# Optimization experiments

Hardware: AMD Instinct MI355X
Metric: run time of the kernel (lower is better)

## Reference

```python
import jax, jax.numpy as jnp
import numpy as np

B, R, H, IN, L = 8, 128, 256, 512, 3
NH, DH = 4, H // 4  # attention heads


def _layernorm(x, g, b, eps=1e-5):
    mu = jnp.mean(x, axis=-1, keepdims=True)
    var = jnp.mean(jnp.square(x - mu), axis=-1, keepdims=True)
    return (x - mu) * jax.lax.rsqrt(var + eps) * g + b


def setup_inputs() -> dict:
    key = jax.random.key(0)
    ks = iter(jax.random.split(key, 40))
    s = 0.02
    d = {}
    d['x'] = jax.random.normal(next(ks), (B, IN), jnp.float32)
    d['We'] = jax.random.normal(next(ks), (IN, H), jnp.float32) * s
    d['be'] = jnp.zeros((H,), jnp.float32)
    # per-graph-layer params, stacked along leading L axis
    d['msg_W1'] = jax.random.normal(next(ks), (L, 2 * H, H), jnp.float32) * s
    d['msg_b1'] = jnp.zeros((L, H), jnp.float32)
    d['msg_W2'] = jax.random.normal(next(ks), (L, H, H), jnp.float32) * s
    d['msg_b2'] = jnp.zeros((L, H), jnp.float32)
    d['upd_W1'] = jax.random.normal(next(ks), (L, 2 * H, H), jnp.float32) * s
    d['upd_b1'] = jnp.zeros((L, H), jnp.float32)
    d['upd_W2'] = jax.random.normal(next(ks), (L, H, H), jnp.float32) * s
    d['upd_b2'] = jnp.zeros((L, H), jnp.float32)
    d['ln_g'] = jnp.ones((L, H), jnp.float32)
    d['ln_b'] = jnp.zeros((L, H), jnp.float32)
    d['rule_adj'] = jax.random.normal(next(ks), (R, R), jnp.float32)
    # multihead attention (4 heads)
    d['Wq'] = jax.random.normal(next(ks), (H, H), jnp.float32) * s
    d['bq'] = jnp.zeros((H,), jnp.float32)
    d['Wk'] = jax.random.normal(next(ks), (H, H), jnp.float32) * s
    d['bk'] = jnp.zeros((H,), jnp.float32)
    d['Wv'] = jax.random.normal(next(ks), (H, H), jnp.float32) * s
    d['bv'] = jnp.zeros((H,), jnp.float32)
    d['Wo'] = jax.random.normal(next(ks), (H, H), jnp.float32) * s
    d['bo'] = jnp.zeros((H,), jnp.float32)
    # readout MLP -> num_rules logits
    d['ro_W1'] = jax.random.normal(next(ks), (H, H), jnp.float32) * s
    d['ro_b1'] = jnp.zeros((H,), jnp.float32)
    d['ro_W2'] = jax.random.normal(next(ks), (H, R), jnp.float32) * s
    d['ro_b2'] = jnp.zeros((R,), jnp.float32)
    return d


def reference(x, We, be, msg_W1, msg_b1, msg_W2, msg_b2,
              upd_W1, upd_b1, upd_W2, upd_b2, ln_g, ln_b, rule_adj,
              Wq, bq, Wk, bk, Wv, bv, Wo, bo,
              ro_W1, ro_b1, ro_W2, ro_b2):
    # node encoder, broadcast to all rule-graph nodes: [B,R,H]
    h0 = x @ We + be
    h = jnp.broadcast_to(h0[:, None, :], (B, R, H))
    # rule adjacency with self-edges excluded (loop used i != j)
    A = jax.nn.sigmoid(rule_adj) * (1.0 - jnp.eye(R, dtype=rule_adj.dtype))  # [R,R]
    for l in range(L):
        # message_net(cat(h_i, h_j)) = relu(h_i@W1a + h_j@W1b + b1)@W2 + b2
        W1a, W1b = msg_W1[l][:H], msg_W1[l][H:]
        a = h @ W1a   # [B,R,H] (receiver i part)
        bb = h @ W1b  # [B,R,H] (sender j part)
        pre = jax.nn.relu(a[:, :, None, :] + bb[:, None, :, :] + msg_b1[l])  # [B,R,R,H]
        m = pre @ msg_W2[l] + msg_b2[l]  # [B,R,R,H] message from j to i
        agg = jnp.einsum('bijh,ij->bih', m, A)  # weighted sum over senders j
        # update_net(cat(h, agg))
        Wu1a, Wu1b = upd_W1[l][:H], upd_W1[l][H:]
        u = jax.nn.relu(h @ Wu1a + agg @ Wu1b + upd_b1[l]) @ upd_W2[l] + upd_b2[l]
        h = _layernorm(h + u, ln_g[l], ln_b[l])
    # multihead self-attention over nodes
    q = (h @ Wq + bq).reshape(B, R, NH, DH)
    k = (h @ Wk + bk).reshape(B, R, NH, DH)
    v = (h @ Wv + bv).reshape(B, R, NH, DH)
    logits = jnp.einsum('bqhd,bkhd->bhqk', q, k) / jnp.sqrt(jnp.float32(DH))
    attn = jax.nn.softmax(logits, axis=-1)
    pooled = jnp.einsum('bhqk,bkhd->bqhd', attn, v).reshape(B, R, H) @ Wo + bo
    g = jnp.mean(pooled, axis=1)  # [B,H]
    rule_logits = jax.nn.relu(g @ ro_W1 + ro_b1) @ ro_W2 + ro_b2
    rule_probabilities = jax.nn.softmax(rule_logits, axis=-1)  # [B,R]
    return rule_probabilities
```

## Files before the change

### kernel.cpp

```cpp
#include <hip/hip_runtime.h>
#include <math.h>

constexpr int NB  = 8;
constexpr int NR  = 128;
constexpr int HID = 256;
constexpr int NIN = 512;
constexpr int DHD = 64;
constexpr size_t SZ = (size_t)NB * NR * HID;

struct KP {
    const float *x, *We, *be, *msg_W1, *msg_b1, *msg_W2, *msg_b2;
    const float *upd_W1, *upd_b1, *upd_W2, *upd_b2, *ln_g, *ln_b, *rule_adj;
    const float *Wq, *bq, *Wk, *bk, *Wv, *bv, *Wo, *bo, *ro_W1, *ro_b1, *ro_W2, *ro_b2;
    float* out;
    float *N0, *N1, *N2;
    float *aB, *bbB, *p1B;
    float *aA, *bbA, *p1A;
    float *W2u, *mb2u, *Aw, *rsum;
    float *mW1s;
    float *h0g;
    float *c0g, *c1g;
    float *gacc;
    float *scratch;
};

__device__ __forceinline__ void gemm_core(
    float (&As)[16][68], float (&Bs)[16][64], int m0, int n0,
    const float* __restrict__ A, const float* __restrict__ B,
    float (&acc)[4][4])
{
    int tid = threadIdx.x;
    int ty = tid >> 4, tx = tid & 15;
    int arow = tid >> 2, acol = (tid & 3) << 2;
    int brow = tid >> 4, bcol = (tid & 15) << 2;
    int m = m0 + arow;

    float4 av = *(const float4*)&A[(size_t)m * HID + acol];
    float4 bv = *(const float4*)&B[(size_t)brow * HID + n0 + bcol];

    for (int k0 = 0; k0 < HID; k0 += 16) {
        As[acol + 0][arow] = av.x;
        As[acol + 1][arow] = av.y;
        As[acol + 2][arow] = av.z;
        As[acol + 3][arow] = av.w;
        *(float4*)&Bs[brow][bcol] = bv;
        __syncthreads();
        if (k0 + 16 < HID) {
            av = *(const float4*)&A[(size_t)m * HID + k0 + 16 + acol];
            bv = *(const float4*)&B[(size_t)(k0 + 16 + brow) * HID + n0 + bcol];
        }
#pragma unroll
        for (int kk = 0; kk < 16; ++kk) {
            float4 af = *(const float4*)&As[kk][ty << 2];
            float4 bf = *(const float4*)&Bs[kk][tx << 2];
            float a_[4] = {af.x, af.y, af.z, af.w};
            float b_[4] = {bf.x, bf.y, bf.z, bf.w};
#pragma unroll
            for (int i = 0; i < 4; ++i)
#pragma unroll
                for (int j = 0; j < 4; ++j) acc[i][j] += a_[i] * b_[j];
        }
        __syncthreads();
    }
}

__device__ __forceinline__ void gemv256w(
    const float* xs, const float* __restrict__ W,
    const float* __restrict__ bias, int relu, float* ys, float* red)
{
    int tid = threadIdx.x;
    int w = tid >> 6, l = tid & 63;
    float4 acc = {0.f, 0.f, 0.f, 0.f};
    const float* Wp = W + (size_t)(w * 64) * HID + l * 4;
    const float* xp = xs + w * 64;
#pragma unroll 16
    for (int kk = 0; kk < 64; ++kk) {
        float xv = xp[kk];
        float4 wv = *(const float4*)(Wp + (size_t)kk * HID);
        acc.x += xv * wv.x; acc.y += xv * wv.y;
        acc.z += xv * wv.z; acc.w += xv * wv.w;
    }
    *(float4*)&red[w * 256 + l * 4] = acc;
    __syncthreads();
    float v = red[tid] + red[256 + tid] + red[512 + tid] + red[768 + tid];
    if (bias) v += bias[tid];
    if (relu) v = fmaxf(v, 0.0f);
    ys[tid] = v;
    __syncthreads();
}

__device__ __forceinline__ void rows4_q(
    const float (&rows)[4][HID], const float* __restrict__ W,
    int col, int q, float o[4])
{
    o[0] = o[1] = o[2] = o[3] = 0.f;
    int kb = q * 64;
#pragma unroll 4
    for (int k0 = 0; k0 < 64; k0 += 4) {
        int k = kb + k0;
        float w0 = W[(size_t)(k + 0) * HID + col];
        float w1 = W[(size_t)(k + 1) * HID + col];
        float w2 = W[(size_t)(k + 2) * HID + col];
        float w3 = W[(size_t)(k + 3) * HID + col];
#pragma unroll
        for (int ii = 0; ii < 4; ++ii) {
            float4 rv = *(const float4*)&rows[ii][k];
            o[ii] += rv.x * w0 + rv.y * w1 + rv.z * w2 + rv.w * w3;
        }
    }
}

__device__ __forceinline__ void rows4_q3(
    const float (&rows)[4][HID],
    const float* __restrict__ W0, const float* __restrict__ W1,
    const float* __restrict__ W2m,
    int col, int q, float o[3][4])
{
#pragma unroll
    for (int p = 0; p < 3; ++p)
#pragma unroll
        for (int ii = 0; ii < 4; ++ii) o[p][ii] = 0.f;
    int kb = q * 64;
#pragma unroll 2
    for (int k0 = 0; k0 < 64; k0 += 4) {
        int k = kb + k0;
        float4 rv[4];
#pragma unroll
        for (int ii = 0; ii < 4; ++ii) rv[ii] = *(const float4*)&rows[ii][k];
        const float* Wp[3] = {W0, W1, W2m};
#pragma unroll
        for (int p = 0; p < 3; ++p) {
            const float* W = Wp[p];
            float w0 = W[(size_t)(k + 0) * HID + col];
            float w1 = W[(size_t)(k + 1) * HID + col];
            float w2 = W[(size_t)(k + 2) * HID + col];
            float w3 = W[(size_t)(k + 3) * HID + col];
#pragma unroll
            for (int ii = 0; ii < 4; ++ii)
                o[p][ii] += rv[ii].x * w0 + rv[ii].y * w1
                          + rv[ii].z * w2 + rv[ii].w * w3;
        }
    }
}

__global__ __launch_bounds__(256) void setup0_kernel(KP P) {
    __shared__ union {
        struct { float As[16][68]; float Bs[16][64]; } g;
        struct { float xs[NIN]; float part[8][32]; } e;
    } L;
    int blk = blockIdx.x;
    int t = threadIdx.x;

    if (blk < 32) {
        int rr = blk * 4 + (t >> 6);
        int l = t & 63;
        float s_loc = 0.f;
#pragma unroll
        for (int rep = 0; rep < 2; ++rep) {
            int j = l + rep * 64;
            float xv = P.rule_adj[rr * NR + j];
            float sg = 1.0f / (1.0f + expf(-xv));
            if (j == rr) sg = 0.0f;
            P.Aw[rr * NR + j] = sg;
            s_loc += sg;
        }
#pragma unroll
        for (int off = 32; off; off >>= 1) s_loc += __shfl_xor(s_loc, off);
        if (l == 0) P.rsum[rr] = s_loc;
    } else if (blk < 80) {
        int idx = blk - 32, l2 = idx >> 4, t16 = idx & 15;
        int m0 = (t16 >> 2) * 64, n0 = (t16 & 3) * 64;
        float acc[4][4] = {};
        gemm_core(L.g.As, L.g.Bs, m0, n0,
                  P.msg_W2 + (size_t)l2 * HID * HID,
                  P.upd_W1 + (size_t)l2 * 2 * HID * HID + (size_t)HID * HID,
                  acc);
        int ty = t >> 4, tx = t & 15;
        float* C = P.W2u + (size_t)l2 * HID * HID;
#pragma unroll
        for (int i = 0; i < 4; ++i) {
            int m = m0 + (ty << 2) + i, n = n0 + (tx << 2);
            float4 o = {acc[i][0], acc[i][1], acc[i][2], acc[i][3]};
            *(float4*)&C[(size_t)m * HID + n] = o;
        }
    } else if (blk < 83) {
        int l2 = blk - 80;
        const float* b2v = P.msg_b2 + l2 * HID;
        const float* Bm = P.upd_W1 + (size_t)l2 * 2 * HID * HID + (size_t)HID * HID;
        float acc = 0.f;
#pragma unroll 4
        for (int k = 0; k < HID; ++k) acc += b2v[k] * Bm[(size_t)k * HID + t];
        P.mb2u[l2 * HID + t] = acc;
    } else if (blk < 147) {
        int idx = blk - 83;
        int b = idx >> 3, s = idx & 7;
        L.e.xs[t]       = P.x[b * NIN + t];
        L.e.xs[256 + t] = P.x[b * NIN + 256 + t];
        __syncthreads();
        int c = t & 31, seg = t >> 5;
        int col = s * 32 + c;
        const float* Wp = P.We + (size_t)(seg * 64) * HID + col;
        const float* xp = L.e.xs + seg * 64;
        float acc = 0.f;
#pragma unroll 16
        for (int k = 0; k < 64; ++k) acc += xp[k] * Wp[(size_t)k * HID];
        L.e.part[seg][c] = acc;
        __syncthreads();
        if (t < 32) {
            float v = 0.f;
#pragma unroll
            for (int sg = 0; sg < 8; ++sg) v += L.e.part[sg][t];
            int cc = s * 32 + t;
            P.h0g[b * HID + cc] = v + P.be[cc];
        }
    } else if (blk < 163) {
        int base = (blk - 147) * 4096;
        for (int i = t; i < 4096; i += 256) {
            int o = base + i;
            P.mW1s[o] = P.msg_W1[o] + P.msg_W1[65536 + o];
        }
    } else {
        int pfid = blk - 163, npf = 256 - 163;
        const float* arr[11] = {P.We, P.msg_W1, P.msg_W2, P.upd_W1, P.upd_W2,
                                P.Wq, P.Wk, P.Wv, P.Wo, P.ro_W1, P.ro_W2};
        const int n4[11] = {32768, 98304, 49152, 98304, 49152,
                            16384, 16384, 16384, 16384, 16384, 8192};
        float s = 0.f;
        for (int a = 0; a < 11; ++a) {
            const float4* p4 = (const float4*)arr[a];
            for (int i = pfid * 256 + t; i < n4[a]; i += npf * 256) {
                float4 v = p4[i];
                s += v.x + v.y + v.z + v.w;
            }
        }
        if (s == 1.0e37f) P.scratch[pfid] = s;
    }
}

__global__ __launch_bounds__(256) void setup1_kernel(KP P) {
    __shared__ float h0s[HID], c0s[HID], p0s[HID], c1s[HID];
    __shared__ float red[1024];
    int b = blockIdx.x;
    int t = threadIdx.x;
    h0s[t] = P.h0g[b * HID + t];
    __syncthreads();
    gemv256w(h0s, P.upd_W1, nullptr, 0, c0s, red);
    gemv256w(h0s, P.mW1s, P.msg_b1, 1, p0s, red);
    gemv256w(p0s, P.W2u, P.mb2u, 0, c1s, red);
    P.c0g[b * HID + t] = c0s[t];
    P.c1g[b * HID + t] = c1s[t];
}

__global__ __launch_bounds__(1024) void layer0p_kernel(KP P) {
    __shared__ float h0s[HID];
    __shared__ float u1s[4][HID];
    __shared__ float nrm[4][HID];
    __shared__ float part3[3][4][4][HID];
    __shared__ float sred[4][4][2];
    int blk = blockIdx.x;
    int m0 = blk * 4;
    int b = m0 >> 7, i0 = m0 & 127;
    int t = threadIdx.x;
    int col = t & 255, q = t >> 8;
    int w4 = (t >> 6) & 3, l = t & 63;

    {
        float c0 = P.c0g[b * HID + col];
        float c1 = P.c1g[b * HID + col];
        if (q == 0) h0s[col] = P.h0g[b * HID + col];
        float ubv = P.upd_b1[col];
        u1s[q][col] = fmaxf(c0 + P.rsum[i0 + q] * c1 + ubv, 0.0f);
    }
    __syncthreads();

    {
        float o[4];
        rows4_q(u1s, P.upd_W2, col, q, o);
#pragma unroll
        for (int ii = 0; ii < 4; ++ii) part3[0][q][ii][col] = o[ii];
    }
    __syncthreads();

    float v;
    {
        float h0v = h0s[col] + P.upd_b2[col];
        v = part3[0][0][q][col] + part3[0][1][q][col]
          + part3[0][2][q][col] + part3[0][3][q][col] + h0v;
        float s = v, qq2 = v * v;
#pragma unroll
        for (int off = 32; off; off >>= 1) {
            s += __shfl_xor(s, off); qq2 += __shfl_xor(qq2, off);
        }
        if (l == 0) { sred[q][w4][0] = s; sred[q][w4][1] = qq2; }
    }
    __syncthreads();
    {
        float ss  = sred[q][0][0] + sred[q][1][0] + sred[q][2][0] + sred[q][3][0];
        float qq2 = sred[q][0][1] + sred[q][1][1] + sred[q][2][1] + sred[q][3][1];
        float mu = ss * (1.0f / HID);
        float inv = rsqrtf(qq2 * (1.0f / HID) - mu * mu + 1e-5f);
        float nv = (v - mu) * inv * P.ln_g[col] + P.ln_b[col];
        nrm[q][col] = nv;
        P.N0[(size_t)(m0 + q) * HID + col] = nv;
    }
    __syncthreads();

    {
        const float* mW1a1 = P.msg_W1 + (size_t)1 * 2 * HID * HID;
        const float* uW1a1 = P.upd_W1 + (size_t)1 * 2 * HID * HID;
        float o3[3][4];
        rows4_q3(nrm, mW1a1, mW1a1 + (size_t)HID * HID, uW1a1, col, q, o3);
#pragma unroll
        for (int p = 0; p < 3; ++p)
#pragma unroll
            for (int ii = 0; ii < 4; ++ii) part3[p][q][ii][col] = o3[p][ii];
    }
    __syncthreads();
    if (q < 3) {
        float* po = (q == 0) ? P.aB : (q == 1) ? P.bbB : P.p1B;
#pragma unroll
        for (int ii = 0; ii < 4; ++ii) {
            float s = part3[q][0][ii][col] + part3[q][1][ii][col]
                    + part3[q][2][ii][col] + part3[q][3][ii][col];
            po[(size_t)(m0 + ii) * HID + col] = s;
        }
    }
}

__global__ __launch_bounds__(1024) void aggproj_kernel(
    const float* __restrict__ a, const float* __restrict__ bbv,
    const float* __restrict__ mb1, const float* __restrict__ Aw,
    const float* __restrict__ rsumv,
    const float* __restrict__ P1, const float* __restrict__ W2u,
    const float* __restrict__ mb2u, const float* __restrict__ ub1,
    const float* __restrict__ uW2, const float* __restrict__ ub2,
    const float* __restrict__ Nprev, const float* __restrict__ lng,
    const float* __restrict__ lnb, float* __restrict__ Nout,
    const float* __restrict__ pw0, const float* __restrict__ pb0, float* __restrict__ o0,
    const float* __restrict__ pw1, const float* __restrict__ pb1, float* __restrict__ o1,
    const float* __restrict__ pw2, const float* __restrict__ pb2, float* __restrict__ o2,
    float* __restrict__ gzero)
{
    __shared__ float ap[4][HID];
    __shared__ float u1s[4][HID];
    __shared__ float nrm[4][HID];
    __shared__ float awr[4][NR];
    __shared__ float part3[3][4][4][HID];
    __shared__ float sred[4][4][2];
    int blk = blockIdx.x;
    int b  = blk >> 5;
    int i0 = (blk & 31) * 4;
    int m0 = b * NR + i0;
    int t  = threadIdx.x;
    int col = t & 255, q = t >> 8;
    int w4 = (t >> 6) & 3, l = t & 63;

    if (gzero && blk == 0 && q == 0) {
#pragma unroll
        for (int i = 0; i < 8; ++i) gzero[i * 256 + col] = 0.f;
    }

    if (t < 512) awr[t >> 7][t & 127] = Aw[(i0 + (t >> 7)) * NR + (t & 127)];

    float bias = mb1[col];
    float ai[4];
#pragma unroll
    for (int ii = 0; ii < 4; ++ii)
        ai[ii] = a[(size_t)(m0 + ii) * HID + col] + bias;
    __syncthreads();

    {
        float acc[4] = {0.f, 0.f, 0.f, 0.f};
        const float* bbb = &bbv[(size_t)b * NR * HID + col];
        int jb = q * 32;
#pragma unroll 4
        for (int j = 0; j < 32; ++j) {
            float bj = bbb[(size_t)(jb + j) * HID];
#pragma unroll
            for (int ii = 0; ii < 4; ++ii) {
                float pre = fmaxf(ai[ii] + bj, 0.0f);
                acc[ii] += awr[ii][jb + j] * pre;
            }
        }
#pragma unroll
        for (int ii = 0; ii < 4; ++ii) part3[0][q][ii][col] = acc[ii];
    }
    __syncthreads();
    ap[q][col] = part3[0][0][q][col] + part3[0][1][q][col]
               + part3[0][2][q][col] + part3[0][3][q][col];
    __syncthreads();

    {
        float o[4];
        rows4_q(ap, W2u, col, q, o);
#pragma unroll
        for (int ii = 0; ii < 4; ++ii) part3[0][q][ii][col] = o[ii];
    }
    __syncthreads();
    {
        float w2f = part3[0][0][q][col] + part3[0][1][q][col]
                  + part3[0][2][q][col] + part3[0][3][q][col];
        float vv = w2f + P1[(size_t)(m0 + q) * HID + col]
                 + rsumv[i0 + q] * mb2u[col] + ub1[col];
        u1s[q][col] = fmaxf(vv, 0.0f);
    }
    __syncthreads();

    {
        float o[4];
        rows4_q(u1s, uW2, col, q, o);
#pragma unroll
        for (int ii = 0; ii < 4; ++ii) part3[0][q][ii][col] = o[ii];
    }
    __syncthreads();
    float v;
    {
        float uf = part3[0][0][q][col] + part3[0][1][q][col]
                 + part3[0][2][q][col] + part3[0][3][q][col];
        v = Nprev[(size_t)(m0 + q) * HID + col] + uf + ub2[col];
        float s = v, qq2 = v * v;
#pragma unroll
        for (int off = 32; off; off >>= 1) {
            s += __shfl_xor(s, off); qq2 += __shfl_xor(qq2, off);
        }
        if (l == 0) { sred[q][w4][0] = s; sred[q][w4][1] = qq2; }
    }
    __syncthreads();
    {
        float ss  = sred[q][0][0] + sred[q][1][0] + sred[q][2][0] + sred[q][3][0];
        float qq2 = sred[q][0][1] + sred[q][1][1] + sred[q][2][1] + sred[q][3][1];
        float mu = ss * (1.0f / HID);
        float inv = rsqrtf(qq2 * (1.0f / HID) - mu * mu + 1e-5f);
        float nv = (v - mu) * inv * lng[col] + lnb[col];
        nrm[q][col] = nv;
        Nout[(size_t)(m0 + q) * HID + col] = nv;
    }
    __syncthreads();

    {
        float o3[3][4];
        rows4_q3(nrm, pw0, pw1, pw2, col, q, o3);
#pragma unroll
        for (int p = 0; p < 3; ++p)
#pragma unroll
            for (int ii = 0; ii < 4; ++ii) part3[p][q][ii][col] = o3[p][ii];
    }
    __syncthreads();
    if (q < 3) {
        const float* pb = (q == 0) ? pb0 : (q == 1) ? pb1 : pb2;
        float* po = (q == 0) ? o0 : (q == 1) ? o1 : o2;
        float pbv = pb ? pb[col] : 0.f;
#pragma unroll
        for (int ii = 0; ii < 4; ++ii) {
            float s = part3[q][0][ii][col] + part3[q][1][ii][col]
                    + part3[q][2][ii][col] + part3[q][3][ii][col] + pbv;
            po[(size_t)(m0 + ii) * HID + col] = s;
        }
    }
}

__global__ __launch_bounds__(256) void attention_kernel(
    const float* __restrict__ q, const float* __restrict__ k,
    const float* __restrict__ v, float* __restrict__ gacc)
{
    __shared__ struct { float KhT[64][128]; float S[16][128]; float qs[16][64]; } L;
    int blk = blockIdx.x;
    int bh = blk >> 3, ig = blk & 7;
    int b = bh >> 2, hd = bh & 3;
    int i0 = ig * 16;
    int t = threadIdx.x;
    const float* qg = q + ((size_t)b * NR) * HID + hd * DHD;
    const float* kg = k + ((size_t)b * NR) * HID + hd * DHD;
    const float* vg = v + ((size_t)b * NR) * HID + hd * DHD;

    {
        int j = t >> 1, half = t & 1;
        const float* krow = kg + (size_t)j * HID + half * 32;
#pragma unroll
        for (int c = 0; c < 32; c += 4) {
            float4 kv = *(const float4*)(krow + c);
            L.KhT[half * 32 + c + 0][j] = kv.x;
            L.KhT[half * 32 + c + 1][j] = kv.y;
            L.KhT[half * 32 + c + 2][j] = kv.z;
            L.KhT[half * 32 + c + 3][j] = kv.w;
        }
    }
    {
        int ii = t >> 4, d0 = (t & 15) * 4;
        *(float4*)&L.qs[ii][d0] = *(const float4*)(qg + (size_t)(i0 + ii) * HID + d0);
    }
    __syncthreads();
    {
        int j = t & 127, ii2 = t >> 7;
        float acc[8] = {0.f,0.f,0.f,0.f,0.f,0.f,0.f,0.f};
#pragma unroll 4
        for (int d = 0; d < 64; ++d) {
            float kv = L.KhT[d][j];
#pragma unroll
            for (int ii = 0; ii < 8; ++ii) acc[ii] += L.qs[ii2 * 8 + ii][d] * kv;
        }
#pragma unroll
        for (int ii = 0; ii < 8; ++ii) L.S[ii2 * 8 + ii][j] = acc[ii] * 0.125f;
    }
    __syncthreads();
    {
        int w = t >> 6, l = t & 63;
#pragma unroll
        for (int r = w * 4; r < w * 4 + 4; ++r) {
            float e0 = L.S[r][l], e1 = L.S[r][l + 64];
            float mx = fmaxf(e0, e1);
#pragma unroll
            for (int off = 32; off; off >>= 1) mx = fmaxf(mx, __shfl_xor(mx, off));
            e0 = expf(e0 - mx); e1 = expf(e1 - mx);
            float sm = e0 + e1;
#pragma unroll
            for (int off = 32; off; off >>= 1) sm += __shfl_xor(sm, off);
            float inv = 1.0f / sm;
            L.S[r][l] = e0 * inv; L.S[r][l + 64] = e1 * inv;
        }
    }
    __syncthreads();
    {
        int d = t & 63, ir = t >> 6;
        float accv[4] = {0.f, 0.f, 0.f, 0.f};
        const float* vp = vg + d;
#pragma unroll 8
        for (int j = 0; j < NR; ++j) {
            float vv = vp[(size_t)j * HID];
#pragma unroll
            for (int p = 0; p < 4; ++p) accv[p] += L.S[p * 4 + ir][j] * vv;
        }
        float s = accv[0] + accv[1] + accv[2] + accv[3];
        atomicAdd(&gacc[b * HID + hd * DHD + d], s);
    }
}

__global__ __launch_bounds__(256) void tailf_kernel(KP P) {
    __shared__ float v0[HID], v1[HID], v2[HID];
    __shared__ float red[1024];
    int b = blockIdx.x;
    int t = threadIdx.x;
    int w = t >> 6, l = t & 63;

    v0[t] = P.gacc[b * HID + t] * (1.0f / NR);
    __syncthreads();
    gemv256w(v0, P.Wo, P.bo, 0, v1, red);
    gemv256w(v1, P.ro_W1, P.ro_b1, 1, v2, red);

    {
        float2 acc = {0.f, 0.f};
        const float* Wp = P.ro_W2 + (size_t)(w * 64) * NR + l * 2;
        const float* xp = v2 + w * 64;
#pragma unroll 8
        for (int kk = 0; kk < 64; ++kk) {
            float xv = xp[kk];
            float2 wv = *(const float2*)(Wp + (size_t)kk * NR);
            acc.x += xv * wv.x; acc.y += xv * wv.y;
        }
        *(float2*)&red[w * 128 + l * 2] = acc;
        __syncthreads();
    }
    float logit = -1e30f;
    if (t < NR) logit = red[t] + red[128 + t] + red[256 + t] + red[384 + t] + P.ro_b2[t];
    __syncthreads();
    float m = logit;
#pragma unroll
    for (int off = 32; off; off >>= 1) m = fmaxf(m, __shfl_xor(m, off));
    if (l == 0) red[w] = m;
    __syncthreads();
    m = fmaxf(red[0], red[1]);
    float e = (t < NR) ? expf(logit - m) : 0.0f;
    float ssum = e;
#pragma unroll
    for (int off = 32; off; off >>= 1) ssum += __shfl_xor(ssum, off);
    if (l == 0) red[4 + w] = ssum;
    __syncthreads();
    float tot = red[4] + red[5];
    if (t < NR) P.out[b * NR + t] = e / tot;
}

extern "C" void kernel_launch(void* const* d_in, const int* in_sizes, int n_in,
                              void* d_out, int out_size, void* d_ws, size_t ws_size,
                              hipStream_t stream)
{
    KP P;
    P.x        = (const float*)d_in[0];
    P.We       = (const float*)d_in[1];
    P.be       = (const float*)d_in[2];
    P.msg_W1   = (const float*)d_in[3];
    P.msg_b1   = (const float*)d_in[4];
    P.msg_W2   = (const float*)d_in[5];
    P.msg_b2   = (const float*)d_in[6];
    P.upd_W1   = (const float*)d_in[7];
    P.upd_b1   = (const float*)d_in[8];
    P.upd_W2   = (const float*)d_in[9];
    P.upd_b2   = (const float*)d_in[10];
    P.ln_g     = (const float*)d_in[11];
    P.ln_b     = (const float*)d_in[12];
    P.rule_adj = (const float*)d_in[13];
    P.Wq       = (const float*)d_in[14];
    P.bq       = (const float*)d_in[15];
    P.Wk       = (const float*)d_in[16];
    P.bk       = (const float*)d_in[17];
    P.Wv       = (const float*)d_in[18];
    P.bv       = (const float*)d_in[19];
    P.Wo       = (const float*)d_in[20];
    P.bo       = (const float*)d_in[21];
    P.ro_W1    = (const float*)d_in[22];
    P.ro_b1    = (const float*)d_in[23];
    P.ro_W2    = (const float*)d_in[24];
    P.ro_b2    = (const float*)d_in[25];
    P.out      = (float*)d_out;

    float* b0 = (float*)d_ws;
    P.N0     = b0;  b0 += SZ;
    P.N1     = b0;  b0 += SZ;
    P.N2     = b0;  b0 += SZ;
    P.aB     = b0;  b0 += SZ;
    P.bbB    = b0;  b0 += SZ;
    P.p1B    = b0;  b0 += SZ;
    P.aA     = b0;  b0 += SZ;
    P.bbA    = b0;  b0 += SZ;
    P.p1A    = b0;  b0 += SZ;
    P.W2u    = b0;  b0 += 3 * HID * HID;
    P.mb2u   = b0;  b0 += 3 * HID;
    P.mW1s   = b0;  b0 += HID * HID;
    P.Aw     = b0;  b0 += NR * NR;
    P.rsum   = b0;  b0 += NR;
    P.h0g    = b0;  b0 += NB * HID;
    P.c0g    = b0;  b0 += NB * HID;
    P.c1g    = b0;  b0 += NB * HID;
    P.gacc   = b0;  b0 += NB * HID;
    P.scratch= b0;  b0 += 256;

    setup0_kernel<<<dim3(256), 256, 0, stream>>>(P);

    setup1_kernel<<<dim3(8), 256, 0, stream>>>(P);

    layer0p_kernel<<<dim3(256), 1024, 0, stream>>>(P);

    {
        const int l = 1;
        const float* mW1a2 = P.msg_W1 + (size_t)2 * 2 * HID * HID;
        const float* uW1a2 = P.upd_W1 + (size_t)2 * 2 * HID * HID;
        aggproj_kernel<<<dim3(256), 1024, 0, stream>>>(
            P.aB, P.bbB, P.msg_b1 + (size_t)l * HID, P.Aw, P.rsum,
            P.p1B, P.W2u + (size_t)l * HID * HID, P.mb2u + l * HID,
            P.upd_b1 + (size_t)l * HID,
            P.upd_W2 + (size_t)l * HID * HID, P.upd_b2 + (size_t)l * HID,
            P.N0, P.ln_g + (size_t)l * HID, P.ln_b + (size_t)l * HID, P.N1,
            mW1a2, nullptr, P.aA,
            mW1a2 + (size_t)HID * HID, nullptr, P.bbA,
            uW1a2, nullptr, P.p1A,
            nullptr);
    }

    {
        const int l = 2;
        aggproj_kernel<<<dim3(256), 1024, 0, stream>>>(
            P.aA, P.bbA, P.msg_b1 + (size_t)l * HID, P.Aw, P.rsum,
            P.p1A, P.W2u + (size_t)l * HID * HID, P.mb2u + l * HID,
            P.upd_b1 + (size_t)l * HID,
            P.upd_W2 + (size_t)l * HID * HID, P.upd_b2 + (size_t)l * HID,
            P.N1, P.ln_g + (size_t)l * HID, P.ln_b + (size_t)l * HID, P.N2,
            P.Wq, P.bq, P.aB,
            P.Wk, P.bk, P.bbB,
            P.Wv, P.bv, P.p1B,
            P.gacc);
    }

    attention_kernel<<<dim3(256), 256, 0, stream>>>(P.aB, P.bbB, P.p1B, P.gacc);

    tailf_kernel<<<dim3(8), 256, 0, stream>>>(P);
}
```

Baseline: 224.5 us.

## Fold setup1 and tail kernels into predecessors via atomic counters

Removes two small kernel launches. setup1 becomes eight extra blocks of setup0 that spin-wait on a global counter until the 163 producer blocks have signalled. The tail readout runs in whichever attention block arrives last for each batch, detected with a per-batch atomic counter. A memset is added to reset the counters. This saves launch gaps and tail overhead, but relies on the producer blocks being co-resident so the spin-wait cannot deadlock.

Result: slower. 239.8 us (+6.9%).

```diff
diff --git a/kernel.cpp b/kernel.cpp
--- a/kernel.cpp
+++ b/kernel.cpp
@@ -22,6 +22,8 @@
     float *c0g, *c1g;
     float *gacc;
     float *scratch;
+    unsigned *cnt0;
+    unsigned *cntA;
 };
 
 __device__ __forceinline__ void gemm_core(
@@ -147,6 +149,8 @@
     __shared__ union {
         struct { float As[16][68]; float Bs[16][64]; } g;
         struct { float xs[NIN]; float part[8][32]; } e;
+        struct { float h0s[HID]; float c0s[HID]; float p0s[HID]; float c1s[HID];
+                 float red[1024]; } hc;
     } L;
     int blk = blockIdx.x;
     int t = threadIdx.x;
@@ -219,8 +223,22 @@
             int o = base + i;
             P.mW1s[o] = P.msg_W1[o] + P.msg_W1[65536 + o];
         }
+    } else if (blk < 171) {
+        int b = blk - 163;
+        if (t == 0) {
+            while (atomicAdd(P.cnt0, 0u) < 163u) __builtin_amdgcn_s_sleep(8);
+            __threadfence();
+        }
+        __syncthreads();
+        L.hc.h0s[t] = P.h0g[b * HID + t];
+        __syncthreads();
+        gemv256w(L.hc.h0s, P.upd_W1, nullptr, 0, L.hc.c0s, L.hc.red);
+        gemv256w(L.hc.h0s, P.mW1s, P.msg_b1, 1, L.hc.p0s, L.hc.red);
+        gemv256w(L.hc.p0s, P.W2u, P.mb2u, 0, L.hc.c1s, L.hc.red);
+        P.c0g[b * HID + t] = L.hc.c0s[t];
+        P.c1g[b * HID + t] = L.hc.c1s[t];
     } else {
-        int pfid = blk - 163, npf = 256 - 163;
+        int pfid = blk - 171, npf = 256 - 171;
         const float* arr[11] = {P.We, P.msg_W1, P.msg_W2, P.upd_W1, P.upd_W2,
                                 P.Wq, P.Wk, P.Wv, P.Wo, P.ro_W1, P.ro_W2};
         const int n4[11] = {32768, 98304, 49152, 98304, 49152,
@@ -235,20 +253,11 @@
         }
         if (s == 1.0e37f) P.scratch[pfid] = s;
     }
-}
-
-__global__ __launch_bounds__(256) void setup1_kernel(KP P) {
-    __shared__ float h0s[HID], c0s[HID], p0s[HID], c1s[HID];
-    __shared__ float red[1024];
-    int b = blockIdx.x;
-    int t = threadIdx.x;
-    h0s[t] = P.h0g[b * HID + t];
-    __syncthreads();
-    gemv256w(h0s, P.upd_W1, nullptr, 0, c0s, red);
-    gemv256w(h0s, P.mW1s, P.msg_b1, 1, p0s, red);
-    gemv256w(p0s, P.W2u, P.mb2u, 0, c1s, red);
-    P.c0g[b * HID + t] = c0s[t];
-    P.c1g[b * HID + t] = c1s[t];
+
+    if (blk < 163) {
+        __syncthreads();
+        if (t == 0) { __threadfence(); atomicAdd(P.cnt0, 1u); }
+    }
 }
 
 __global__ __launch_bounds__(1024) void layer0p_kernel(KP P) {
@@ -459,19 +468,21 @@
     }
 }
 
-__global__ __launch_bounds__(256) void attention_kernel(
-    const float* __restrict__ q, const float* __restrict__ k,
-    const float* __restrict__ v, float* __restrict__ gacc)
+__global__ __launch_bounds__(256) void attention_kernel(KP P)
 {
-    __shared__ struct { float KhT[64][128]; float S[16][128]; float qs[16][64]; } L;
+    __shared__ union {
+        struct { float KhT[64][128]; float S[16][128]; float qs[16][64]; } a;
+        struct { float v0[HID]; float v1[HID]; float v2[HID]; float red[1024]; } tl;
+    } L;
+    __shared__ int last;
     int blk = blockIdx.x;
     int bh = blk >> 3, ig = blk & 7;
     int b = bh >> 2, hd = bh & 3;
     int i0 = ig * 16;
     int t = threadIdx.x;
-    const float* qg = q + ((size_t)b * NR) * HID + hd * DHD;
-    const float* kg = k + ((size_t)b * NR) * HID + hd * DHD;
-    const float* vg = v + ((size_t)b * NR) * HID + hd * DHD;
+    const float* qg = P.aB  + ((size_t)b * NR) * HID + hd * DHD;
+    const float* kg = P.bbB + ((size_t)b * NR) * HID + hd * DHD;
+    const float* vg = P.p1B + ((size_t)b * NR) * HID + hd * DHD;
 
     {
         int j = t >> 1, half = t & 1;
@@ -479,15 +490,15 @@
 #pragma unroll
         for (int c = 0; c < 32; c += 4) {
             float4 kv = *(const float4*)(krow + c);
-            L.KhT[half * 32 + c + 0][j] = kv.x;
-            L.KhT[half * 32 + c + 1][j] = kv.y;
-            L.KhT[half * 32 + c + 2][j] = kv.z;
-            L.KhT[half * 32 + c + 3][j] = kv.w;
+            L.a.KhT[half * 32 + c + 0][j] = kv.x;
+            L.a.KhT[half * 32 + c + 1][j] = kv.y;
+            L.a.KhT[half * 32 + c + 2][j] = kv.z;
+            L.a.KhT[half * 32 + c + 3][j] = kv.w;
         }
     }
     {
         int ii = t >> 4, d0 = (t & 15) * 4;
-        *(float4*)&L.qs[ii][d0] = *(const float4*)(qg + (size_t)(i0 + ii) * HID + d0);
+        *(float4*)&L.a.qs[ii][d0] = *(const float4*)(qg + (size_t)(i0 + ii) * HID + d0);
     }
     __syncthreads();
     {
@@ -495,19 +506,19 @@
         float acc[8] = {0.f,0.f,0.f,0.f,0.f,0.f,0.f,0.f};
 #pragma unroll 4
         for (int d = 0; d < 64; ++d) {
-            float kv = L.KhT[d][j];
-#pragma unroll
-            for (int ii = 0; ii < 8; ++ii) acc[ii] += L.qs[ii2 * 8 + ii][d] * kv;
-        }
-#pragma unroll
-        for (int ii = 0; ii < 8; ++ii) L.S[ii2 * 8 + ii][j] = acc[ii] * 0.125f;
+            float kv = L.a.KhT[d][j];
+#pragma unroll
+            for (int ii = 0; ii < 8; ++ii) acc[ii] += L.a.qs[ii2 * 8 + ii][d] * kv;
+        }
+#pragma unroll
+        for (int ii = 0; ii < 8; ++ii) L.a.S[ii2 * 8 + ii][j] = acc[ii] * 0.125f;
     }
     __syncthreads();
     {
         int w = t >> 6, l = t & 63;
 #pragma unroll
         for (int r = w * 4; r < w * 4 + 4; ++r) {
-            float e0 = L.S[r][l], e1 = L.S[r][l + 64];
+            float e0 = L.a.S[r][l], e1 = L.a.S[r][l + 64];
             float mx = fmaxf(e0, e1);
 #pragma unroll
             for (int off = 32; off; off >>= 1) mx = fmaxf(mx, __shfl_xor(mx, off));
@@ -516,7 +527,7 @@
 #pragma unroll
             for (int off = 32; off; off >>= 1) sm += __shfl_xor(sm, off);
             float inv = 1.0f / sm;
-            L.S[r][l] = e0 * inv; L.S[r][l + 64] = e1 * inv;
+            L.a.S[r][l] = e0 * inv; L.a.S[r][l + 64] = e1 * inv;
         }
     }
     __syncthreads();
@@ -528,54 +539,59 @@
         for (int j = 0; j < NR; ++j) {
             float vv = vp[(size_t)j * HID];
 #pragma unroll
-            for (int p = 0; p < 4; ++p) accv[p] += L.S[p * 4 + ir][j] * vv;
+            for (int p = 0; p < 4; ++p) accv[p] += L.a.S[p * 4 + ir][j] * vv;
         }
         float s = accv[0] + accv[1] + accv[2] + accv[3];
-        atomicAdd(&gacc[b * HID + hd * DHD + d], s);
-    }
-}
-
-__global__ __launch_bounds__(256) void tailf_kernel(KP P) {
-    __shared__ float v0[HID], v1[HID], v2[HID];
-    __shared__ float red[1024];
-    int b = blockIdx.x;
-    int t = threadIdx.x;
+        atomicAdd(&P.gacc[b * HID + hd * DHD + d], s);
+    }
+
+    __threadfence();
+    __syncthreads();
+    if (t == 0) {
+        unsigned old = atomicAdd(&P.cntA[b], 1u);
+        last = (old == 31u) ? 1 : 0;
+    }
+    __syncthreads();
+    if (!last) return;
+    __threadfence();
+    __syncthreads();
+
     int w = t >> 6, l = t & 63;
-
-    v0[t] = P.gacc[b * HID + t] * (1.0f / NR);
-    __syncthreads();
-    gemv256w(v0, P.Wo, P.bo, 0, v1, red);
-    gemv256w(v1, P.ro_W1, P.ro_b1, 1, v2, red);
+    L.tl.v0[t] = P.gacc[b * HID + t] * (1.0f / NR);
+    __syncthreads();
+    gemv256w(L.tl.v0, P.Wo, P.bo, 0, L.tl.v1, L.tl.red);
+    gemv256w(L.tl.v1, P.ro_W1, P.ro_b1, 1, L.tl.v2, L.tl.red);
 
     {
         float2 acc = {0.f, 0.f};
         const float* Wp = P.ro_W2 + (size_t)(w * 64) * NR + l * 2;
-        const float* xp = v2 + w * 64;
+        const float* xp = L.tl.v2 + w * 64;
 #pragma unroll 8
         for (int kk = 0; kk < 64; ++kk) {
             float xv = xp[kk];
             float2 wv = *(const float2*)(Wp + (size_t)kk * NR);
             acc.x += xv * wv.x; acc.y += xv * wv.y;
         }
-        *(float2*)&red[w * 128 + l * 2] = acc;
+        *(float2*)&L.tl.red[w * 128 + l * 2] = acc;
         __syncthreads();
     }
     float logit = -1e30f;
-    if (t < NR) logit = red[t] + red[128 + t] + red[256 + t] + red[384 + t] + P.ro_b2[t];
+    if (t < NR) logit = L.tl.red[t] + L.tl.red[128 + t] + L.tl.red[256 + t]
+                      + L.tl.red[384 + t] + P.ro_b2[t];
     __syncthreads();
     float m = logit;
 #pragma unroll
     for (int off = 32; off; off >>= 1) m = fmaxf(m, __shfl_xor(m, off));
-    if (l == 0) red[w] = m;
-    __syncthreads();
-    m = fmaxf(red[0], red[1]);
+    if (l == 0) L.tl.red[w] = m;
+    __syncthreads();
+    m = fmaxf(L.tl.red[0], L.tl.red[1]);
     float e = (t < NR) ? expf(logit - m) : 0.0f;
     float ssum = e;
 #pragma unroll
     for (int off = 32; off; off >>= 1) ssum += __shfl_xor(ssum, off);
-    if (l == 0) red[4 + w] = ssum;
-    __syncthreads();
-    float tot = red[4] + red[5];
+    if (l == 0) L.tl.red[4 + w] = ssum;
+    __syncthreads();
+    float tot = L.tl.red[4] + L.tl.red[5];
     if (t < NR) P.out[b * NR + t] = e / tot;
 }
 
@@ -632,10 +648,13 @@
     P.c1g    = b0;  b0 += NB * HID;
     P.gacc   = b0;  b0 += NB * HID;
     P.scratch= b0;  b0 += 256;
+    P.cnt0   = (unsigned*)b0;
+    P.cntA   = (unsigned*)b0 + 8;
+    b0 += 64;
+
+    hipMemsetAsync((void*)P.cnt0, 0, 64 * sizeof(float), stream);
 
     setup0_kernel<<<dim3(256), 256, 0, stream>>>(P);
-
-    setup1_kernel<<<dim3(8), 256, 0, stream>>>(P);
 
     layer0p_kernel<<<dim3(256), 1024, 0, stream>>>(P);
 
@@ -669,7 +688,5 @@
             P.gacc);
     }
 
-    attention_kernel<<<dim3(256), 256, 0, stream>>>(P.aB, P.bbB, P.p1B, P.gacc);
-
-    tailf_kernel<<<dim3(8), 256, 0, stream>>>(P);
-}
+    attention_kernel<<<dim3(256), 256, 0, stream>>>(P);
+}
```
